# Optimization experiments

Hardware: AMD Instinct MI355X
Metric: run time of the kernel (lower is better)

## Reference

```python
import jax, jax.numpy as jnp
import numpy as np

N, C, F, T, H = 8, 64, 256, 256, 64


def _ln(x, g, b, eps=1e-5):
    m = x.mean(-1, keepdims=True)
    v = x.var(-1, keepdims=True)  # biased var, matches torch LayerNorm
    return (x - m) * jax.lax.rsqrt(v + eps) * g + b


def setup_inputs() -> dict:
    key = jax.random.key(0)
    ks = jax.random.split(key, 8)
    s = 1.0 / np.sqrt(C)
    return {
        "inputs": jax.random.normal(ks[0], (N, C, F, T), jnp.float32),
        "Wq": jax.random.normal(ks[1], (H, C), jnp.float32) * s,
        "bq": jnp.zeros((H,), jnp.float32),
        "Wk": jax.random.normal(ks[2], (H, C), jnp.float32) * s,
        "bk": jnp.zeros((H,), jnp.float32),
        "Wv": jax.random.normal(ks[3], (H, C), jnp.float32) * s,
        "bv": jnp.zeros((H,), jnp.float32),
        "g1": jnp.ones((C,), jnp.float32),
        "b1": jnp.zeros((C,), jnp.float32),
        "g2": jnp.ones((H,), jnp.float32),
        "b2": jnp.zeros((H,), jnp.float32),
        "Wt": jax.random.normal(ks[4], (C, H), jnp.float32) * s,
        "bt": jnp.zeros((C,), jnp.float32),
        "g3": jnp.ones((C,), jnp.float32),
        "b3": jnp.zeros((C,), jnp.float32),
        "alpha": jnp.full((1,), 0.25, jnp.float32),
    }


def reference(inputs, Wq, bq, Wk, bk, Wv, bv, g1, b1, g2, b2, Wt, bt, g3, b3, alpha):
    n, c, f, t = inputs.shape
    # [N,C,F,T] -> [N*T, F, C]: attention over freq bins, channels as features
    x = inputs.transpose(0, 3, 2, 1).reshape(n * t, f, c)
    h = _ln(x, g1, b1)
    q = h @ Wq.T + bq  # [B, F, H]
    k = h @ Wk.T + bk
    v = h @ Wv.T + bv
    scale = 1.0 / jnp.sqrt(jnp.asarray(q.shape[-1], q.dtype))
    e = jnp.einsum('bth,bsh->bts', q, k) * scale  # [B, F, F]
    a = jax.nn.softmax(e, axis=-1)
    wv = jnp.einsum('bts,bsh->bth', a, v)
    wv = _ln(wv, g2, b2)
    out = wv @ Wt.T + bt  # [B, F, C]
    out = out.reshape(n, t, f, c)
    out = _ln(out, g3, b3)  # LayerNorm over channel dim
    out = jnp.where(out >= 0, out, alpha * out)  # PReLU (single param)
    out = out.transpose(0, 3, 2, 1)  # back to [N, C, F, T]
    return out + inputs  # dropout is identity in eval mode
```

## Files before the change

kernel.cpp:

```cpp
#include <hip/hip_runtime.h>

typedef _Float16 f16;
typedef _Float16 f16x2 __attribute__((ext_vector_type(2)));
typedef _Float16 f16x8 __attribute__((ext_vector_type(8)));
typedef float f32x16 __attribute__((ext_vector_type(16)));
typedef unsigned int u32;
typedef unsigned short u16;

#define MFMA(a, b, c) __builtin_amdgcn_mfma_f32_32x32x16_f16((a), (b), (c), 0, 0, 0)

__device__ __forceinline__ u32 pk2(float a, float b) {
  union { f16x2 h; u32 u; } x;
  x.h[0] = (f16)a; x.h[1] = (f16)b;
  return x.u;
}
__device__ __forceinline__ float2 up2(u32 u) {
  union { u32 u_; f16x2 h; } x; x.u_ = u;
  return make_float2((float)x.h[0], (float)x.h[1]);
}
__device__ __forceinline__ f16x8 mk8(u32 a, u32 b, u32 c, u32 d) {
  union { u32 u[4]; f16x8 v; } x;
  x.u[0] = a; x.u[1] = b; x.u[2] = c; x.u[3] = d;
  return x.v;
}
__device__ __forceinline__ u16 f16b(float v) {
  union { f16 h; u16 u; } x; x.h = (f16)v; return x.u;
}
__device__ __forceinline__ float ex2(float x) {
#if __has_builtin(__builtin_amdgcn_exp2f)
  return __builtin_amdgcn_exp2f(x);
#else
  return exp2f(x);
#endif
}

__device__ __forceinline__ void sp2(float a, float b, float S, u32* hi, u32* lo) {
  union { f16x2 h; u32 u; } xh, xl;
  xh.h[0] = (f16)a; xh.h[1] = (f16)b;
  float ra = (a - (float)xh.h[0]) * S;
  float rb = (b - (float)xh.h[1]) * S;
  xl.h[0] = (f16)ra; xl.h[1] = (f16)rb;
  *hi = xh.u; *lo = xl.u;
}

template<int CTRL>
__device__ __forceinline__ float dpp_add(float v) {
  int t = __builtin_amdgcn_update_dpp(0, __builtin_bit_cast(int, v), CTRL, 0xF, 0xF, true);
  return v + __builtin_bit_cast(float, t);
}
__device__ __forceinline__ float red32(float v) {
  v = dpp_add<0xB1>(v);
  v = dpp_add<0x4E>(v);
  v = dpp_add<0x141>(v);
  v = dpp_add<0x140>(v);
  int sw = __builtin_amdgcn_ds_swizzle(__builtin_bit_cast(int, v), 0x401F);
  return v + __builtin_bit_cast(float, sw);
}

__device__ __forceinline__ void xfrag2(const f32x16 a, int kt1, int g5,
                                       f16x8* hi, f16x8* lo, float S) {
  u32 uh[4], ul[4];
#pragma unroll
  for (int j = 0; j < 4; ++j) {
    float v0 = kt1 ? a[8 + 2 * j] : a[2 * j];
    float v1 = kt1 ? a[9 + 2 * j] : a[2 * j + 1];
    sp2(v0, v1, S, &uh[j], &ul[j]);
  }
  u32 sh[4], sl[4];
#pragma unroll
  for (int j = 0; j < 4; ++j) {
    sh[j] = (u32)__shfl_xor((int)uh[j], 32);
    sl[j] = (u32)__shfl_xor((int)ul[j], 32);
  }
  *hi = mk8(g5 ? sh[2] : uh[0], g5 ? sh[3] : uh[1],
            g5 ? uh[2] : sh[0], g5 ? uh[3] : sh[1]);
  *lo = mk8(g5 ? sl[2] : ul[0], g5 ? sl[3] : ul[1],
            g5 ? ul[2] : sl[0], g5 ? ul[3] : sl[1]);
}

__device__ __forceinline__ f16x8 ldfrag(const char* plane, int row, int kt, int g5) {
  int s = row & 15;
  int c8 = 4 * kt + 2 * g5;
  uint2 a = *(const uint2*)(plane + row * 128 + ((c8) ^ s) * 8);
  uint2 b = *(const uint2*)(plane + row * 128 + ((c8 + 1) ^ s) * 8);
  return mk8(a.x, a.y, b.x, b.y);
}

__global__ __launch_bounds__(256) void k_pre32(const float* __restrict__ inp,
                                               float* __restrict__ xws) {
  __shared__ float tile[64 * 65];
  const int bid = blockIdx.x;
  const int n = bid >> 10;
  const int rem = bid & 1023;
  const int f = rem >> 2;
  const int t0 = (rem & 3) << 6;
  const int tid = threadIdx.x;

  const int tt = tid & 63, cb = tid >> 6;
  const float* src = inp + ((size_t)n * 64 * 256 + f) * 256 + t0;
#pragma unroll
  for (int k = 0; k < 16; ++k) {
    int c = cb * 16 + k;
    tile[c * 65 + tt] = src[(size_t)c * 65536 + tt];
  }
  __syncthreads();
  const int c2 = (tid & 31) * 2, tb = tid >> 5;
#pragma unroll
  for (int k = 0; k < 8; ++k) {
    int t = tb + 8 * k;
    float2 v = make_float2(tile[c2 * 65 + t], tile[(c2 + 1) * 65 + t]);
    *(float2*)(xws + ((size_t)(n * 256 + t0 + t) * 256 + f) * 64 + c2) = v;
  }
}

__global__ __launch_bounds__(512, 2) void k_attn(
    const float* __restrict__ xg,
    u16* __restrict__ yws,
    const float* __restrict__ Wq, const float* __restrict__ bq,
    const float* __restrict__ Wk, const float* __restrict__ bk,
    const float* __restrict__ Wv, const float* __restrict__ bv,
    const float* __restrict__ g1, const float* __restrict__ b1,
    const float* __restrict__ g2, const float* __restrict__ b2,
    const float* __restrict__ Wt, const float* __restrict__ bt,
    const float* __restrict__ g3, const float* __restrict__ b3,
    const float* __restrict__ alp) {
  extern __shared__ char smem[];
  char* Khi = smem;
  char* Klo = smem + 32768;
  char* Vlds = smem + 65536;
  char* WkH = smem + 98304;
  char* WkL = smem + 106496;
  char* WvH = smem + 114688;
  char* WvL = smem + 122880;
  char* WqH = smem + 131072;
  char* WqL = smem + 139264;
  char* WtH = smem + 147456;

  const int tid = threadIdx.x;
  const int w = tid >> 6;
  const int lane = tid & 63;
  const int l31 = lane & 31;
  const int g5 = lane >> 5;
  const int l7 = l31 & 7;
  const int b = blockIdx.x;
  const float* xb = xg + (size_t)b * 16384;
  const float RLO = 1.f / 512.f;

  float xv[32];
  {
    int f = 32 * w + l31;
#pragma unroll
    for (int kt = 0; kt < 4; ++kt) {
      float4 a = *(const float4*)(xb + f * 64 + 16 * kt + 8 * g5);
      float4 c = *(const float4*)(xb + f * 64 + 16 * kt + 8 * g5 + 4);
      xv[kt * 8 + 0] = a.x; xv[kt * 8 + 1] = a.y;
      xv[kt * 8 + 2] = a.z; xv[kt * 8 + 3] = a.w;
      xv[kt * 8 + 4] = c.x; xv[kt * 8 + 5] = c.y;
      xv[kt * 8 + 6] = c.z; xv[kt * 8 + 7] = c.w;
    }
  }

  {
    const int prow = tid >> 3, pc = tid & 7;
    const int ps = prow & 15;
    const int pha = (2 * pc) ^ ps, phb = (2 * pc + 1) ^ ps;
    const size_t off = (size_t)prow * 64 + pc * 8;
    {
      float4 a = *(const float4*)(Wk + off);
      float4 c = *(const float4*)(Wk + off + 4);
      u32 h0, l0, h1, l1, h2, l2, h3, l3;
      sp2(a.x, a.y, 512.f, &h0, &l0); sp2(a.z, a.w, 512.f, &h1, &l1);
      sp2(c.x, c.y, 512.f, &h2, &l2); sp2(c.z, c.w, 512.f, &h3, &l3);
      *(uint2*)(WkH + prow * 128 + pha * 8) = make_uint2(h0, h1);
      *(uint2*)(WkH + prow * 128 + phb * 8) = make_uint2(h2, h3);
      *(uint2*)(WkL + prow * 128 + pha * 8) = make_uint2(l0, l1);
      *(uint2*)(WkL + prow * 128 + phb * 8) = make_uint2(l2, l3);
    }
    {
      float4 a = *(const float4*)(Wv + off);
      float4 c = *(const float4*)(Wv + off + 4);
      u32 h0, l0, h1, l1, h2, l2, h3, l3;
      sp2(a.x, a.y, 512.f, &h0, &l0); sp2(a.z, a.w, 512.f, &h1, &l1);
      sp2(c.x, c.y, 512.f, &h2, &l2); sp2(c.z, c.w, 512.f, &h3, &l3);
      *(uint2*)(WvH + prow * 128 + pha * 8) = make_uint2(h0, h1);
      *(uint2*)(WvH + prow * 128 + phb * 8) = make_uint2(h2, h3);
      *(uint2*)(WvL + prow * 128 + pha * 8) = make_uint2(l0, l1);
      *(uint2*)(WvL + prow * 128 + phb * 8) = make_uint2(l2, l3);
    }
    {
      float4 a = *(const float4*)(Wq + off);
      float4 c = *(const float4*)(Wq + off + 4);
      u32 h0, l0, h1, l1, h2, l2, h3, l3;
      sp2(a.x, a.y, 512.f, &h0, &l0); sp2(a.z, a.w, 512.f, &h1, &l1);
      sp2(c.x, c.y, 512.f, &h2, &l2); sp2(c.z, c.w, 512.f, &h3, &l3);
      *(uint2*)(WqH + prow * 128 + pha * 8) = make_uint2(h0, h1);
      *(uint2*)(WqH + prow * 128 + phb * 8) = make_uint2(h2, h3);
      *(uint2*)(WqL + prow * 128 + pha * 8) = make_uint2(l0, l1);
      *(uint2*)(WqL + prow * 128 + phb * 8) = make_uint2(l2, l3);
    }
    {
      float4 a = *(const float4*)(Wt + off);
      float4 c = *(const float4*)(Wt + off + 4);
      *(uint2*)(WtH + prow * 128 + pha * 8) = make_uint2(pk2(a.x, a.y), pk2(a.z, a.w));
      *(uint2*)(WtH + prow * 128 + phb * 8) = make_uint2(pk2(c.x, c.y), pk2(c.z, c.w));
    }
  }
  __syncthreads();

  f16x8 hhi[4], hlo[4];
  {
    float s = 0.f, sq = 0.f;
#pragma unroll
    for (int i = 0; i < 32; ++i) { s += xv[i]; sq += xv[i] * xv[i]; }
    s += __shfl_xor(s, 32);
    sq += __shfl_xor(sq, 32);
    float mean = s * (1.f / 64.f);
    float var = sq * (1.f / 64.f) - mean * mean;
    float rs = rsqrtf(var + 1e-5f);
#pragma unroll
    for (int kt = 0; kt < 4; ++kt) {
      int c0 = 16 * kt + 8 * g5;
      u32 ph[4], pl[4];
#pragma unroll
      for (int j = 0; j < 4; ++j) {
        float v0 = (xv[kt * 8 + 2 * j] - mean) * rs * g1[c0 + 2 * j] + b1[c0 + 2 * j];
        float v1 = (xv[kt * 8 + 2 * j + 1] - mean) * rs * g1[c0 + 2 * j + 1] + b1[c0 + 2 * j + 1];
        sp2(v0, v1, 512.f, &ph[j], &pl[j]);
      }
      hhi[kt] = mk8(ph[0], ph[1], ph[2], ph[3]);
      hlo[kt] = mk8(pl[0], pl[1], pl[2], pl[3]);
    }
  }

  {
    f32x16 ah[2] = {}, al[2] = {};
#pragma unroll
    for (int kt = 0; kt < 4; ++kt) {
#pragma unroll
      for (int ot = 0; ot < 2; ++ot) {
        f16x8 mh = ldfrag(WkH, l31 + 32 * ot, kt, g5);
        f16x8 ml = ldfrag(WkL, l31 + 32 * ot, kt, g5);
        ah[ot] = MFMA(mh, hhi[kt], ah[ot]);
        al[ot] = MFMA(mh, hlo[kt], al[ot]);
        al[ot] = MFMA(ml, hhi[kt], al[ot]);
      }
    }
    int fk = 32 * w + l31;
    int sw = l7;
#pragma unroll
    for (int ot = 0; ot < 2; ++ot) {
#pragma unroll
      for (int rq = 0; rq < 4; ++rq) {
        int o0 = 32 * ot + 8 * rq + 4 * g5;
        float4 bb = *(const float4*)(bk + o0);
        float k0 = ah[ot][4 * rq + 0] + al[ot][4 * rq + 0] * RLO + bb.x;
        float k1 = ah[ot][4 * rq + 1] + al[ot][4 * rq + 1] * RLO + bb.y;
        float k2 = ah[ot][4 * rq + 2] + al[ot][4 * rq + 2] * RLO + bb.z;
        float k3 = ah[ot][4 * rq + 3] + al[ot][4 * rq + 3] * RLO + bb.w;
        u32 h01, l01, h23, l23;
        sp2(k0, k1, 512.f, &h01, &l01);
        sp2(k2, k3, 512.f, &h23, &l23);
        int ch = (4 * ot + rq) ^ sw;
        *(uint2*)(Khi + fk * 128 + ch * 16 + 8 * g5) = make_uint2(h01, h23);
        *(uint2*)(Klo + fk * 128 + ch * 16 + 8 * g5) = make_uint2(l01, l23);
      }
    }
  }

  {
    f32x16 ah[2] = {}, al[2] = {};
#pragma unroll
    for (int kt = 0; kt < 4; ++kt) {
#pragma unroll
      for (int nt = 0; nt < 2; ++nt) {
        f16x8 mh = ldfrag(WvH, l31 + 32 * nt, kt, g5);
        f16x8 ml = ldfrag(WvL, l31 + 32 * nt, kt, g5);
        ah[nt] = MFMA(hhi[kt], mh, ah[nt]);
        al[nt] = MFMA(hlo[kt], mh, al[nt]);
        al[nt] = MFMA(hhi[kt], ml, al[nt]);
      }
    }
#pragma unroll
    for (int nt = 0; nt < 2; ++nt) {
      int hh = l31 + 32 * nt;
      float bvj = bv[hh];
      int sw = hh & 7;
#pragma unroll
      for (int rq = 0; rq < 4; ++rq) {
        float v0 = ah[nt][4 * rq + 0] + al[nt][4 * rq + 0] * RLO + bvj;
        float v1 = ah[nt][4 * rq + 1] + al[nt][4 * rq + 1] * RLO + bvj;
        float v2 = ah[nt][4 * rq + 2] + al[nt][4 * rq + 2] * RLO + bvj;
        float v3 = ah[nt][4 * rq + 3] + al[nt][4 * rq + 3] * RLO + bvj;
        int ch = (4 * w + rq) ^ sw;
        *(uint2*)(Vlds + hh * 512 + ch * 16 + 8 * g5) =
            make_uint2(pk2(v0, v1), pk2(v2, v3));
      }
    }
  }

  f16x8 qf[4], ql[4];
  {
    f32x16 ah[2] = {}, al[2] = {};
#pragma unroll
    for (int kt = 0; kt < 4; ++kt) {
#pragma unroll
      for (int ot = 0; ot < 2; ++ot) {
        f16x8 mh = ldfrag(WqH, l31 + 32 * ot, kt, g5);
        f16x8 ml = ldfrag(WqL, l31 + 32 * ot, kt, g5);
        ah[ot] = MFMA(mh, hhi[kt], ah[ot]);
        al[ot] = MFMA(mh, hlo[kt], al[ot]);
        al[ot] = MFMA(ml, hhi[kt], al[ot]);
      }
    }
    const float qs = 0.18033688011112042f;
#pragma unroll
    for (int ot = 0; ot < 2; ++ot) {
#pragma unroll
      for (int rq = 0; rq < 4; ++rq) {
        int o0 = 32 * ot + 8 * rq + 4 * g5;
        float4 bb = *(const float4*)(bq + o0);
        ah[ot][4 * rq + 0] = (ah[ot][4 * rq + 0] + al[ot][4 * rq + 0] * RLO + bb.x) * qs;
        ah[ot][4 * rq + 1] = (ah[ot][4 * rq + 1] + al[ot][4 * rq + 1] * RLO + bb.y) * qs;
        ah[ot][4 * rq + 2] = (ah[ot][4 * rq + 2] + al[ot][4 * rq + 2] * RLO + bb.z) * qs;
        ah[ot][4 * rq + 3] = (ah[ot][4 * rq + 3] + al[ot][4 * rq + 3] * RLO + bb.w) * qs;
      }
    }
#pragma unroll
    for (int kt = 0; kt < 4; ++kt)
      xfrag2(ah[kt >> 1], kt & 1, g5, &qf[kt], &ql[kt], 512.f);
  }

  __syncthreads();

  const float alv = alp[0];
  const float btc0 = bt[l31], btc1 = bt[l31 + 32];
  const float g3v0 = g3[l31], g3v1 = g3[l31 + 32];
  const float b3v0 = b3[l31], b3v1 = b3[l31 + 32];
  u16* yb = yws + (size_t)b * 16384;

  f32x16 e[8];
#pragma unroll
  for (int m = 0; m < 8; ++m) {
    const char* krh = Khi + (l31 + 32 * m) * 128;
    const char* krl = Klo + (l31 + 32 * m) * 128;
    f32x16 eh = {}, em = {};
#pragma unroll
    for (int kt = 0; kt < 4; ++kt) {
      int ch = (2 * kt + g5) ^ l7;
      f16x8 kh = __builtin_bit_cast(f16x8, *(const uint4*)(krh + ch * 16));
      f16x8 kl = __builtin_bit_cast(f16x8, *(const uint4*)(krl + ch * 16));
      eh = MFMA(kh, qf[kt], eh);
      em = MFMA(kh, ql[kt], em);
      em = MFMA(kl, qf[kt], em);
    }
#pragma unroll
    for (int r = 0; r < 16; ++r) e[m][r] = eh[r] + em[r] * RLO;
  }
  float mx = -3.0e38f;
#pragma unroll
  for (int m = 0; m < 8; ++m)
#pragma unroll
    for (int r = 0; r < 16; ++r) mx = fmaxf(mx, e[m][r]);
  mx = fmaxf(mx, __shfl_xor(mx, 32));
  float s = 0.f;
#pragma unroll
  for (int m = 0; m < 8; ++m)
#pragma unroll
    for (int r = 0; r < 16; ++r) {
      float p = ex2(e[m][r] - mx);
      e[m][r] = p;
      s += p;
    }
  s += __shfl_xor(s, 32);
  float rcps = 1.0f / s;

  f32x16 wv0h = {}, wv0l = {}, wv1h = {}, wv1l = {};
#pragma unroll
  for (int kt = 0; kt < 16; ++kt) {
    f16x8 ph, pl;
    xfrag2(e[kt >> 1], kt & 1, g5, &ph, &pl, 512.f);
    int ch = (2 * kt + g5) ^ l7;
    f16x8 vaf = __builtin_bit_cast(f16x8, *(const uint4*)(Vlds + l31 * 512 + ch * 16));
    wv0h = MFMA(vaf, ph, wv0h);
    wv0l = MFMA(vaf, pl, wv0l);
    f16x8 vbf = __builtin_bit_cast(f16x8, *(const uint4*)(Vlds + (l31 + 32) * 512 + ch * 16));
    wv1h = MFMA(vbf, ph, wv1h);
    wv1l = MFMA(vbf, pl, wv1l);
  }

  f32x16 wv0, wv1;
  float s2 = 0.f, sq2 = 0.f;
#pragma unroll
  for (int r = 0; r < 16; ++r) {
    float a = (wv0h[r] + wv0l[r] * RLO) * rcps; wv0[r] = a; s2 += a; sq2 += a * a;
    float c = (wv1h[r] + wv1l[r] * RLO) * rcps; wv1[r] = c; s2 += c; sq2 += c * c;
  }
  s2 += __shfl_xor(s2, 32);
  sq2 += __shfl_xor(sq2, 32);
  float m2 = s2 * (1.f / 64.f);
  float v2 = sq2 * (1.f / 64.f) - m2 * m2;
  float rs2 = rsqrtf(v2 + 1e-5f);
#pragma unroll
  for (int at = 0; at < 2; ++at) {
#pragma unroll
    for (int rq = 0; rq < 4; ++rq) {
      int h0 = 32 * at + 8 * rq + 4 * g5;
      float4 gg = *(const float4*)(g2 + h0);
      float4 bb = *(const float4*)(b2 + h0);
      f32x16& a = at ? wv1 : wv0;
      a[4 * rq + 0] = (a[4 * rq + 0] - m2) * rs2 * gg.x + bb.x;
      a[4 * rq + 1] = (a[4 * rq + 1] - m2) * rs2 * gg.y + bb.y;
      a[4 * rq + 2] = (a[4 * rq + 2] - m2) * rs2 * gg.z + bb.z;
      a[4 * rq + 3] = (a[4 * rq + 3] - m2) * rs2 * gg.w + bb.w;
    }
  }
  f16x8 afh[4], afl[4];
  xfrag2(wv0, 0, g5, &afh[0], &afl[0], 1.f);
  xfrag2(wv0, 1, g5, &afh[1], &afl[1], 1.f);
  xfrag2(wv1, 0, g5, &afh[2], &afl[2], 1.f);
  xfrag2(wv1, 1, g5, &afh[3], &afl[3], 1.f);

  f32x16 o0 = {}, o1 = {};
#pragma unroll
  for (int kt = 0; kt < 4; ++kt) {
    f16x8 w0 = ldfrag(WtH, l31, kt, g5);
    f16x8 w1 = ldfrag(WtH, l31 + 32, kt, g5);
    o0 = MFMA(afh[kt], w0, o0);
    o0 = MFMA(afl[kt], w0, o0);
    o1 = MFMA(afh[kt], w1, o1);
    o1 = MFMA(afl[kt], w1, o1);
  }

  const int fbase = 32 * w + 4 * g5;
#pragma unroll
  for (int r = 0; r < 16; ++r) {
    float v0 = o0[r] + btc0;
    float v1 = o1[r] + btc1;
    float S = red32(v0 + v1);
    float SQ = red32(v0 * v0 + v1 * v1);
    float m3 = S * (1.f / 64.f);
    float va = SQ * (1.f / 64.f) - m3 * m3;
    float rs3 = rsqrtf(va + 1e-5f);
    float y0 = (v0 - m3) * rs3 * g3v0 + b3v0;
    float y1 = (v1 - m3) * rs3 * g3v1 + b3v1;
    y0 = y0 >= 0.f ? y0 : alv * y0;
    y1 = y1 >= 0.f ? y1 : alv * y1;
    int f = fbase + (r & 3) + 8 * (r >> 2);
    u16* yp = yb + f * 64 + l31;
    yp[0] = f16b(y0);
    yp[32] = f16b(y1);
  }
}

__global__ __launch_bounds__(256) void k_post(const float* __restrict__ inp,
                                              const u16* __restrict__ yws,
                                              float* __restrict__ out) {
  __shared__ float tile[64 * 66];
  const int bid = blockIdx.x;
  const int n = bid >> 10;
  const int rem = bid & 1023;
  const int f = rem >> 2;
  const int t0 = (rem & 3) << 6;
  const int tid = threadIdx.x;

  const int c2 = (tid & 31) * 2, tb = tid >> 5;
  const u32* src = (const u32*)yws;
#pragma unroll
  for (int k = 0; k < 8; ++k) {
    int t = tb + 8 * k;
    u32 v = src[((n * 256 + t0 + t) * 256 + f) * 32 + (tid & 31)];
    float2 p = up2(v);
    tile[t * 66 + c2] = p.x;
    tile[t * 66 + c2 + 1] = p.y;
  }
  __syncthreads();
  const int tt = tid & 63, cb = tid >> 6;
#pragma unroll
  for (int k = 0; k < 16; ++k) {
    int c = cb * 16 + k;
    size_t idx = ((size_t)(n * 64 + c) * 256 + f) * 256 + t0 + tt;
    out[idx] = inp[idx] + tile[tt * 66 + c];
  }
}

extern "C" void kernel_launch(void* const* d_in, const int* in_sizes, int n_in,
                              void* d_out, int out_size, void* d_ws, size_t ws_size,
                              hipStream_t stream) {
  const float* inp = (const float*)d_in[0];
  const float* Wq = (const float*)d_in[1];
  const float* bq = (const float*)d_in[2];
  const float* Wk = (const float*)d_in[3];
  const float* bk = (const float*)d_in[4];
  const float* Wv = (const float*)d_in[5];
  const float* bv = (const float*)d_in[6];
  const float* g1 = (const float*)d_in[7];
  const float* b1 = (const float*)d_in[8];
  const float* g2 = (const float*)d_in[9];
  const float* b2 = (const float*)d_in[10];
  const float* Wt = (const float*)d_in[11];
  const float* bt = (const float*)d_in[12];
  const float* g3 = (const float*)d_in[13];
  const float* b3 = (const float*)d_in[14];
  const float* al = (const float*)d_in[15];
  float* xstage = (float*)d_out;
  u16* yws = (u16*)d_ws;

  (void)hipFuncSetAttribute((const void*)k_attn,
                            hipFuncAttributeMaxDynamicSharedMemorySize, 155648);
  k_pre32<<<8192, 256, 0, stream>>>(inp, xstage);
  k_attn<<<2048, 512, 155648, stream>>>(xstage, yws, Wq, bq, Wk, bk, Wv, bv,
                                        g1, b1, g2, b2, Wt, bt, g3, b3, al);
  k_post<<<8192, 256, 0, stream>>>(inp, yws, (float*)d_out);
}
```

Measured before the change: 310.4 us.

## Drop hi/lo split for P·V and pad K/V LDS row strides

The P·V product now uses a single fp16 conversion of the softmax probabilities instead of a hi/lo split pair, which halves the MFMAs and conversion work in that loop. The K and V LDS rows are also padded (136 and 520 byte strides), presumably to reduce bank conflicts. The padding raises dynamic LDS from 155648 to 160256 bytes, which may exceed the per-CU budget for two 512-thread blocks and cut occupancy. The padded strides also break the 16-byte XOR swizzle alignment, and the single fp16 probability path loses some precision.

```diff
diff --git a/kernel.cpp b/kernel.cpp
--- a/kernel.cpp
+++ b/kernel.cpp
@@ -8,6 +8,9 @@
 typedef unsigned short u16;
 
 #define MFMA(a, b, c) __builtin_amdgcn_mfma_f32_32x32x16_f16((a), (b), (c), 0, 0, 0)
+
+#define KSTRIDE 136
+#define VSTRIDE 520
 
 __device__ __forceinline__ u32 pk2(float a, float b) {
   union { f16x2 h; u32 u; } x;
@@ -55,6 +58,26 @@
   v = dpp_add<0x140>(v);
   int sw = __builtin_amdgcn_ds_swizzle(__builtin_bit_cast(int, v), 0x401F);
   return v + __builtin_bit_cast(float, sw);
+}
+
+__device__ __forceinline__ f16x8 xfrag(const f32x16 a, int kt1, int g5) {
+  u32 u0, u1, u2, u3;
+  if (kt1 == 0) {
+    u0 = pk2(a[0], a[1]);   u1 = pk2(a[2], a[3]);
+    u2 = pk2(a[4], a[5]);   u3 = pk2(a[6], a[7]);
+  } else {
+    u0 = pk2(a[8], a[9]);   u1 = pk2(a[10], a[11]);
+    u2 = pk2(a[12], a[13]); u3 = pk2(a[14], a[15]);
+  }
+  u32 s0 = (u32)__shfl_xor((int)u0, 32);
+  u32 s1 = (u32)__shfl_xor((int)u1, 32);
+  u32 s2 = (u32)__shfl_xor((int)u2, 32);
+  u32 s3 = (u32)__shfl_xor((int)u3, 32);
+  u32 r0 = g5 ? s2 : u0;
+  u32 r1 = g5 ? s3 : u1;
+  u32 r2 = g5 ? u2 : s0;
+  u32 r3 = g5 ? u3 : s1;
+  return mk8(r0, r1, r2, r3);
 }
 
 __device__ __forceinline__ void xfrag2(const f32x16 a, int kt1, int g5,
@@ -126,15 +149,15 @@
     const float* __restrict__ alp) {
   extern __shared__ char smem[];
   char* Khi = smem;
-  char* Klo = smem + 32768;
-  char* Vlds = smem + 65536;
-  char* WkH = smem + 98304;
-  char* WkL = smem + 106496;
-  char* WvH = smem + 114688;
-  char* WvL = smem + 122880;
-  char* WqH = smem + 131072;
-  char* WqL = smem + 139264;
-  char* WtH = smem + 147456;
+  char* Klo = smem + 34816;
+  char* Vlds = smem + 69632;
+  char* WkH = smem + 102912;
+  char* WkL = smem + 111104;
+  char* WvH = smem + 119296;
+  char* WvL = smem + 127488;
+  char* WqH = smem + 135680;
+  char* WqL = smem + 143872;
+  char* WtH = smem + 152064;
 
   const int tid = threadIdx.x;
   const int w = tid >> 6;
@@ -261,8 +284,8 @@
         sp2(k0, k1, 512.f, &h01, &l01);
         sp2(k2, k3, 512.f, &h23, &l23);
         int ch = (4 * ot + rq) ^ sw;
-        *(uint2*)(Khi + fk * 128 + ch * 16 + 8 * g5) = make_uint2(h01, h23);
-        *(uint2*)(Klo + fk * 128 + ch * 16 + 8 * g5) = make_uint2(l01, l23);
+        *(uint2*)(Khi + fk * KSTRIDE + ch * 16 + 8 * g5) = make_uint2(h01, h23);
+        *(uint2*)(Klo + fk * KSTRIDE + ch * 16 + 8 * g5) = make_uint2(l01, l23);
       }
     }
   }
@@ -292,7 +315,7 @@
         float v2 = ah[nt][4 * rq + 2] + al[nt][4 * rq + 2] * RLO + bvj;
         float v3 = ah[nt][4 * rq + 3] + al[nt][4 * rq + 3] * RLO + bvj;
         int ch = (4 * w + rq) ^ sw;
-        *(uint2*)(Vlds + hh * 512 + ch * 16 + 8 * g5) =
+        *(uint2*)(Vlds + hh * VSTRIDE + ch * 16 + 8 * g5) =
             make_uint2(pk2(v0, v1), pk2(v2, v3));
       }
     }
@@ -341,8 +364,8 @@
   f32x16 e[8];
 #pragma unroll
   for (int m = 0; m < 8; ++m) {
-    const char* krh = Khi + (l31 + 32 * m) * 128;
-    const char* krl = Klo + (l31 + 32 * m) * 128;
+    const char* krh = Khi + (l31 + 32 * m) * KSTRIDE;
+    const char* krl = Klo + (l31 + 32 * m) * KSTRIDE;
     f32x16 eh = {}, em = {};
 #pragma unroll
     for (int kt = 0; kt < 4; ++kt) {
@@ -374,26 +397,22 @@
   s += __shfl_xor(s, 32);
   float rcps = 1.0f / s;
 
-  f32x16 wv0h = {}, wv0l = {}, wv1h = {}, wv1l = {};
+  f32x16 wv0 = {}, wv1 = {};
 #pragma unroll
   for (int kt = 0; kt < 16; ++kt) {
-    f16x8 ph, pl;
-    xfrag2(e[kt >> 1], kt & 1, g5, &ph, &pl, 512.f);
+    f16x8 pf = xfrag(e[kt >> 1], kt & 1, g5);
     int ch = (2 * kt + g5) ^ l7;
-    f16x8 vaf = __builtin_bit_cast(f16x8, *(const uint4*)(Vlds + l31 * 512 + ch * 16));
-    wv0h = MFMA(vaf, ph, wv0h);
-    wv0l = MFMA(vaf, pl, wv0l);
-    f16x8 vbf = __builtin_bit_cast(f16x8, *(const uint4*)(Vlds + (l31 + 32) * 512 + ch * 16));
-    wv1h = MFMA(vbf, ph, wv1h);
-    wv1l = MFMA(vbf, pl, wv1l);
-  }
-
-  f32x16 wv0, wv1;
+    f16x8 vaf = __builtin_bit_cast(f16x8, *(const uint4*)(Vlds + l31 * VSTRIDE + ch * 16));
+    wv0 = MFMA(vaf, pf, wv0);
+    f16x8 vbf = __builtin_bit_cast(f16x8, *(const uint4*)(Vlds + (l31 + 32) * VSTRIDE + ch * 16));
+    wv1 = MFMA(vbf, pf, wv1);
+  }
+
   float s2 = 0.f, sq2 = 0.f;
 #pragma unroll
   for (int r = 0; r < 16; ++r) {
-    float a = (wv0h[r] + wv0l[r] * RLO) * rcps; wv0[r] = a; s2 += a; sq2 += a * a;
-    float c = (wv1h[r] + wv1l[r] * RLO) * rcps; wv1[r] = c; s2 += c; sq2 += c * c;
+    float a = wv0[r] * rcps; wv0[r] = a; s2 += a; sq2 += a * a;
+    float c = wv1[r] * rcps; wv1[r] = c; s2 += c; sq2 += c * c;
   }
   s2 += __shfl_xor(s2, 32);
   sq2 += __shfl_xor(sq2, 32);
@@ -506,9 +525,9 @@
   u16* yws = (u16*)d_ws;
 
   (void)hipFuncSetAttribute((const void*)k_attn,
-                            hipFuncAttributeMaxDynamicSharedMemorySize, 155648);
+                            hipFuncAttributeMaxDynamicSharedMemorySize, 160256);
   k_pre32<<<8192, 256, 0, stream>>>(inp, xstage);
-  k_attn<<<2048, 512, 155648, stream>>>(xstage, yws, Wq, bq, Wk, bk, Wv, bv,
+  k_attn<<<2048, 512, 160256, stream>>>(xstage, yws, Wq, bq, Wk, bk, Wv, bv,
                                         g1, b1, g2, b2, Wt, bt, g3, b3, al);
   k_post<<<8192, 256, 0, stream>>>(inp, yws, (float*)d_out);
 }
```

Result: slower. 406.4 us (+30.9%).
